# Performance work log

Measured on AMD Instinct MI355X. Metric: run time of the kernel, lower is better.

The kernel has to match this reference:

```python
import jax, jax.numpy as jnp
import numpy as np

BC = 256      # block_channel
RC = 64       # reduced_channel = BC // 4
NB0, NB1 = 4, 3   # num_blocks per modality (1024/256, 768/256)
TB = NB0 + NB1    # total_blocks
EPS = 1e-5        # BatchNorm eps (eval mode, running_mean=0, running_var=1)
LOWEST = 0.0      # lowest_atten


def setup_inputs() -> dict:
    key = jax.random.key(0)
    k = jax.random.split(key, 4)
    B, T = 8, 4096
    x0 = jax.random.normal(k[0], (B, 1024, T), jnp.float32)
    x1 = jax.random.normal(k[1], (B, 768, T), jnp.float32)
    W1 = jax.random.normal(k[2], (BC, RC), jnp.float32) / np.sqrt(BC).astype(np.float32)
    b1 = jnp.zeros((RC,), jnp.float32)
    gamma = jnp.ones((RC,), jnp.float32)
    beta = jnp.zeros((RC,), jnp.float32)
    Wh = jax.random.normal(k[3], (TB, RC, BC), jnp.float32) / np.sqrt(RC).astype(np.float32)
    bh = jnp.zeros((TB, BC), jnp.float32)
    return {"x0": x0, "x1": x1, "W1": W1, "b1": b1, "gamma": gamma,
            "beta": beta, "Wh": Wh, "bh": bh}


def reference(x0, x1, W1, b1, gamma, beta, Wh, bh):
    B, _, T = x0.shape
    # split channels into blocks: [B, nb, BC, T]
    xr0 = x0.reshape(B, NB0, BC, T)
    xr1 = x1.reshape(B, NB1, BC, T)
    # block-sum over blocks, then global average pool over time -> [B, BC]
    gap = xr0.sum(axis=1).mean(axis=-1) + xr1.sum(axis=1).mean(axis=-1)
    # joint projector: Linear -> BatchNorm1d(eval: mean=0, var=1) -> ReLU
    h = gap @ W1 + b1
    h = jnp.maximum(h * (gamma / jnp.sqrt(1.0 + EPS)) + beta, 0.0)  # [B, RC]
    # all TB attention heads as one grouped GEMM: [TB, B, BC]
    scores = jnp.einsum('br,krc->kbc', h, Wh) + bh[:, None, :]
    att = jax.nn.softmax(scores, axis=0)          # softmax over block axis (dim=0)
    att = jnp.transpose(att, (1, 0, 2))           # [B, TB, BC]
    att = LOWEST + att * (1.0 - LOWEST)
    # scale each block's features
    out0 = (xr0 * att[:, :NB0, :, None]).reshape(x0.shape)
    out1 = (xr1 * att[:, NB0:, :, None]).reshape(x1.shape)
    return (out0, out1)
```

## Files before the change

kernel.cpp:

```cpp
#include <hip/hip_runtime.h>
#include <hip/hip_bf16.h>

#define B_SZ 8
#define T_SZ 4096
#define BC 256
#define RC 64
#define NB0 4
#define NB1 3
#define TB 7
#define ROWS0 (B_SZ * 1024)
#define ROWS1 (B_SZ * 768)
#define ROWS_TOTAL (ROWS0 + ROWS1)
#define X0_ELEMS (33554432ull)

__global__ __launch_bounds__(256) void gap_kernel(const float* __restrict__ x0,
                                                  const float* __restrict__ x1,
                                                  float* __restrict__ gap) {
    const int gtid = blockIdx.x * blockDim.x + threadIdx.x;
    const int wave = gtid >> 6;
    const int lane = threadIdx.x & 63;

    const float4* src;
    int b, c;
    if (wave < ROWS0) {
        b = wave >> 10;
        const int ch = wave & 1023;
        c = ch & 255;
        src = (const float4*)(x0 + (size_t)wave * T_SZ);
    } else {
        const int r = wave - ROWS0;
        b = r / 768;
        const int ch = r - b * 768;
        c = ch & 255;
        src = (const float4*)(x1 + (size_t)r * T_SZ);
    }

    float sum = 0.0f;
#pragma unroll
    for (int it = 0; it < 16; ++it) {
        float4 v = src[it * 64 + lane];
        sum += (v.x + v.y) + (v.z + v.w);
    }
#pragma unroll
    for (int off = 32; off > 0; off >>= 1)
        sum += __shfl_down(sum, off, 64);

    if (lane == 0)
        atomicAdd(gap + b * BC + c, sum * (1.0f / (float)T_SZ));
}

__global__ __launch_bounds__(256) void attn_kernel(const float* __restrict__ gap,
                                                   const float* __restrict__ W1,
                                                   const float* __restrict__ b1,
                                                   const float* __restrict__ gamma,
                                                   const float* __restrict__ beta,
                                                   const float* __restrict__ Wh,
                                                   const float* __restrict__ bh,
                                                   float* __restrict__ att) {
    __shared__ float s_gap[B_SZ][BC];
    __shared__ float s_h[B_SZ][RC];
    const int tid = threadIdx.x;

#pragma unroll
    for (int b = 0; b < B_SZ; ++b)
        s_gap[b][tid] = gap[b * BC + tid];
    __syncthreads();

    const float bnscale = rsqrtf(1.0f + 1e-5f);
    for (int p = tid; p < B_SZ * RC; p += 256) {
        const int b = p >> 6;
        const int r = p & 63;
        float acc = 0.0f;
        for (int c = 0; c < BC; ++c)
            acc = fmaf(s_gap[b][c], W1[c * RC + r], acc);
        acc += b1[r];
        acc = acc * (gamma[r] * bnscale) + beta[r];
        s_h[b][r] = fmaxf(acc, 0.0f);
    }
    __syncthreads();

    float sc[TB];
#pragma unroll 1
    for (int b = 0; b < B_SZ; ++b) {
        float mx = -1e30f;
#pragma unroll
        for (int k = 0; k < TB; ++k) {
            float acc = bh[k * BC + tid];
            for (int r = 0; r < RC; ++r)
                acc = fmaf(s_h[b][r], Wh[(k * RC + r) * BC + tid], acc);
            sc[k] = acc;
            mx = fmaxf(mx, acc);
        }
        float sum = 0.0f;
#pragma unroll
        for (int k = 0; k < TB; ++k) {
            sc[k] = __expf(sc[k] - mx);
            sum += sc[k];
        }
        const float inv = 1.0f / sum;
#pragma unroll
        for (int k = 0; k < TB; ++k)
            att[(b * TB + k) * BC + tid] = sc[k] * inv;
    }
}

__global__ __launch_bounds__(256) void scale_kernel(const float* __restrict__ x0,
                                                    const float* __restrict__ x1,
                                                    const float* __restrict__ att,
                                                    float* __restrict__ out) {
    const int row = blockIdx.x;
    const float4* src;
    float4* dst;
    float a;
    if (row < ROWS0) {
        const int b = row >> 10;
        const int ch = row & 1023;
        a = att[(b * TB + (ch >> 8)) * BC + (ch & 255)];
        src = (const float4*)(x0 + (size_t)row * T_SZ);
        dst = (float4*)(out + (size_t)row * T_SZ);
    } else {
        const int r = row - ROWS0;
        const int b = r / 768;
        const int ch = r - b * 768;
        a = att[(b * TB + NB0 + (ch >> 8)) * BC + (ch & 255)];
        src = (const float4*)(x1 + (size_t)r * T_SZ);
        dst = (float4*)(out + X0_ELEMS + (size_t)r * T_SZ);
    }
    const int tid = threadIdx.x;
#pragma unroll
    for (int it = 0; it < 4; ++it) {
        float4 v = src[it * 256 + tid];
        v.x *= a; v.y *= a; v.z *= a; v.w *= a;
        dst[it * 256 + tid] = v;
    }
}

extern "C" void kernel_launch(void* const* d_in, const int* in_sizes, int n_in,
                              void* d_out, int out_size, void* d_ws, size_t ws_size,
                              hipStream_t stream) {
    const float* x0    = (const float*)d_in[0];
    const float* x1    = (const float*)d_in[1];
    const float* W1    = (const float*)d_in[2];
    const float* b1    = (const float*)d_in[3];
    const float* gamma = (const float*)d_in[4];
    const float* beta  = (const float*)d_in[5];
    const float* Wh    = (const float*)d_in[6];
    const float* bh    = (const float*)d_in[7];
    float* out = (float*)d_out;

    float* gap = (float*)d_ws;
    float* att = gap + 2048;

    hipMemsetAsync(gap, 0, B_SZ * BC * sizeof(float), stream);

    gap_kernel<<<ROWS_TOTAL / 4, 256, 0, stream>>>(x0, x1, gap);
    attn_kernel<<<1, 256, 0, stream>>>(gap, W1, b1, gamma, beta, Wh, bh, att);
    scale_kernel<<<ROWS_TOTAL, 256, 0, stream>>>(x0, x1, att, out);
}
```

Measured before the change: 469.6 us.

## Replace atomic GAP with per-row sums, parallelize attention over batch, nontemporal stores

The pooling kernel now writes one mean per row into a workspace buffer instead of atomically accumulating into a shared gap array, which also removes the memset launch. The attention kernel runs one block per batch item, sums the block rows itself, and splits the first projection across four thread groups with a shared-memory reduction, replacing a single serial block. The scale kernel uses nontemporal stores for the large output write to reduce cache pollution. The workload stays dominated by memory traffic over x, so the gains are expected mainly from shortening the serial attention step and the launch overhead.

Result: slower. 580.8 us (+23.7%).

```diff
diff --git a/kernel.cpp b/kernel.cpp
--- a/kernel.cpp
+++ b/kernel.cpp
@@ -13,32 +13,23 @@
 #define ROWS_TOTAL (ROWS0 + ROWS1)
 #define X0_ELEMS (33554432ull)
 
-__global__ __launch_bounds__(256) void gap_kernel(const float* __restrict__ x0,
-                                                  const float* __restrict__ x1,
-                                                  float* __restrict__ gap) {
+typedef float vfloat4 __attribute__((ext_vector_type(4)));
+
+__global__ __launch_bounds__(256) void rowsum_kernel(const float* __restrict__ x0,
+                                                     const float* __restrict__ x1,
+                                                     float* __restrict__ rowsum) {
     const int gtid = blockIdx.x * blockDim.x + threadIdx.x;
-    const int wave = gtid >> 6;
+    const int row  = gtid >> 6;
     const int lane = threadIdx.x & 63;
 
-    const float4* src;
-    int b, c;
-    if (wave < ROWS0) {
-        b = wave >> 10;
-        const int ch = wave & 1023;
-        c = ch & 255;
-        src = (const float4*)(x0 + (size_t)wave * T_SZ);
-    } else {
-        const int r = wave - ROWS0;
-        b = r / 768;
-        const int ch = r - b * 768;
-        c = ch & 255;
-        src = (const float4*)(x1 + (size_t)r * T_SZ);
-    }
+    const vfloat4* src = (row < ROWS0)
+        ? (const vfloat4*)(x0 + (size_t)row * T_SZ)
+        : (const vfloat4*)(x1 + (size_t)(row - ROWS0) * T_SZ);
 
     float sum = 0.0f;
 #pragma unroll
     for (int it = 0; it < 16; ++it) {
-        float4 v = src[it * 64 + lane];
+        vfloat4 v = src[it * 64 + lane];
         sum += (v.x + v.y) + (v.z + v.w);
     }
 #pragma unroll
@@ -46,10 +37,10 @@
         sum += __shfl_down(sum, off, 64);
 
     if (lane == 0)
-        atomicAdd(gap + b * BC + c, sum * (1.0f / (float)T_SZ));
+        rowsum[row] = sum * (1.0f / (float)T_SZ);
 }
 
-__global__ __launch_bounds__(256) void attn_kernel(const float* __restrict__ gap,
+__global__ __launch_bounds__(256) void attn_kernel(const float* __restrict__ rowsum,
                                                    const float* __restrict__ W1,
                                                    const float* __restrict__ b1,
                                                    const float* __restrict__ gamma,
@@ -57,51 +48,64 @@
                                                    const float* __restrict__ Wh,
                                                    const float* __restrict__ bh,
                                                    float* __restrict__ att) {
-    __shared__ float s_gap[B_SZ][BC];
-    __shared__ float s_h[B_SZ][RC];
+    __shared__ float s_gap[BC];
+    __shared__ float s_part[256];
+    __shared__ float s_h[RC];
+
+    const int b   = blockIdx.x;
     const int tid = threadIdx.x;
 
+    float g = 0.0f;
 #pragma unroll
-    for (int b = 0; b < B_SZ; ++b)
-        s_gap[b][tid] = gap[b * BC + tid];
+    for (int nb = 0; nb < NB0; ++nb)
+        g += rowsum[b * 1024 + nb * BC + tid];
+#pragma unroll
+    for (int nb = 0; nb < NB1; ++nb)
+        g += rowsum[ROWS0 + b * 768 + nb * BC + tid];
+    s_gap[tid] = g;
     __syncthreads();
 
-    const float bnscale = rsqrtf(1.0f + 1e-5f);
-    for (int p = tid; p < B_SZ * RC; p += 256) {
-        const int b = p >> 6;
-        const int r = p & 63;
+    {
+        const int r = tid & 63;
+        const int q = tid >> 6;
         float acc = 0.0f;
-        for (int c = 0; c < BC; ++c)
-            acc = fmaf(s_gap[b][c], W1[c * RC + r], acc);
-        acc += b1[r];
-        acc = acc * (gamma[r] * bnscale) + beta[r];
-        s_h[b][r] = fmaxf(acc, 0.0f);
+#pragma unroll
+        for (int i = 0; i < 64; ++i) {
+            const int c = q * 64 + i;
+            acc = fmaf(s_gap[c], W1[c * RC + r], acc);
+        }
+        s_part[tid] = acc;
+    }
+    __syncthreads();
+    if (tid < RC) {
+        float acc = s_part[tid] + s_part[tid + 64] + s_part[tid + 128] + s_part[tid + 192];
+        acc += b1[tid];
+        acc = acc * (gamma[tid] * rsqrtf(1.0f + 1e-5f)) + beta[tid];
+        s_h[tid] = fmaxf(acc, 0.0f);
     }
     __syncthreads();
 
     float sc[TB];
-#pragma unroll 1
-    for (int b = 0; b < B_SZ; ++b) {
-        float mx = -1e30f;
+    float mx = -1e30f;
 #pragma unroll
-        for (int k = 0; k < TB; ++k) {
-            float acc = bh[k * BC + tid];
-            for (int r = 0; r < RC; ++r)
-                acc = fmaf(s_h[b][r], Wh[(k * RC + r) * BC + tid], acc);
-            sc[k] = acc;
-            mx = fmaxf(mx, acc);
-        }
-        float sum = 0.0f;
+    for (int k = 0; k < TB; ++k) {
+        float acc = bh[k * BC + tid];
 #pragma unroll
-        for (int k = 0; k < TB; ++k) {
-            sc[k] = __expf(sc[k] - mx);
-            sum += sc[k];
-        }
-        const float inv = 1.0f / sum;
+        for (int r = 0; r < RC; ++r)
+            acc = fmaf(s_h[r], Wh[(k * RC + r) * BC + tid], acc);
+        sc[k] = acc;
+        mx = fmaxf(mx, acc);
+    }
+    float sum = 0.0f;
 #pragma unroll
-        for (int k = 0; k < TB; ++k)
-            att[(b * TB + k) * BC + tid] = sc[k] * inv;
+    for (int k = 0; k < TB; ++k) {
+        sc[k] = __expf(sc[k] - mx);
+        sum += sc[k];
     }
+    const float inv = 1.0f / sum;
+#pragma unroll
+    for (int k = 0; k < TB; ++k)
+        att[(b * TB + k) * BC + tid] = sc[k] * inv;
 }
 
 __global__ __launch_bounds__(256) void scale_kernel(const float* __restrict__ x0,
@@ -109,29 +113,29 @@
                                                     const float* __restrict__ att,
                                                     float* __restrict__ out) {
     const int row = blockIdx.x;
-    const float4* src;
-    float4* dst;
+    const vfloat4* src;
+    vfloat4* dst;
     float a;
     if (row < ROWS0) {
         const int b = row >> 10;
         const int ch = row & 1023;
         a = att[(b * TB + (ch >> 8)) * BC + (ch & 255)];
-        src = (const float4*)(x0 + (size_t)row * T_SZ);
-        dst = (float4*)(out + (size_t)row * T_SZ);
+        src = (const vfloat4*)(x0 + (size_t)row * T_SZ);
+        dst = (vfloat4*)(out + (size_t)row * T_SZ);
     } else {
         const int r = row - ROWS0;
         const int b = r / 768;
         const int ch = r - b * 768;
         a = att[(b * TB + NB0 + (ch >> 8)) * BC + (ch & 255)];
-        src = (const float4*)(x1 + (size_t)r * T_SZ);
-        dst = (float4*)(out + X0_ELEMS + (size_t)r * T_SZ);
+        src = (const vfloat4*)(x1 + (size_t)r * T_SZ);
+        dst = (vfloat4*)(out + X0_ELEMS + (size_t)r * T_SZ);
     }
     const int tid = threadIdx.x;
 #pragma unroll
     for (int it = 0; it < 4; ++it) {
-        float4 v = src[it * 256 + tid];
-        v.x *= a; v.y *= a; v.z *= a; v.w *= a;
-        dst[it * 256 + tid] = v;
+        vfloat4 v = src[it * 256 + tid];
+        v *= a;
+        __builtin_nontemporal_store(v, &dst[it * 256 + tid]);
     }
 }
 
@@ -148,12 +152,10 @@
     const float* bh    = (const float*)d_in[7];
     float* out = (float*)d_out;
 
-    float* gap = (float*)d_ws;
-    float* att = gap + 2048;
+    float* rowsum = (float*)d_ws;
+    float* att    = rowsum + ROWS_TOTAL;
 
-    hipMemsetAsync(gap, 0, B_SZ * BC * sizeof(float), stream);
-
-    gap_kernel<<<ROWS_TOTAL / 4, 256, 0, stream>>>(x0, x1, gap);
-    attn_kernel<<<1, 256, 0, stream>>>(gap, W1, b1, gamma, beta, Wh, bh, att);
+    rowsum_kernel<<<ROWS_TOTAL / 4, 256, 0, stream>>>(x0, x1, rowsum);
+    attn_kernel<<<B_SZ, 256, 0, stream>>>(rowsum, W1, b1, gamma, beta, Wh, bh, att);
     scale_kernel<<<ROWS_TOTAL, 256, 0, stream>>>(x0, x1, att, out);
 }
```
